# Kernel optimization log

Hardware: AMD Instinct MI355X
Metric: run time of the kernel (lower is better)

Reference implementation:

```python
import jax, jax.numpy as jnp
import numpy as np

B = 2          # graphs (images)
GRID = 13      # patches per spatial dim -> N = 169 patches per image
N = GRID * GRID
NN = B * N     # total nodes
C = 256        # hidden_dim / out_channels per head
H = 4          # attention heads
L = 3          # GAT layers
LRELU_SLOPE = 0.2
LN_EPS = 1e-5


def _dense_edges():
    # fully-connected directed graph (i != j) per image, as in create_graph
    idx = np.arange(N)
    src, dst = np.meshgrid(idx, idx, indexing='ij')
    mask = src != dst
    src, dst = src[mask], dst[mask]              # [N*(N-1)]
    offs = (np.arange(B) * N)[:, None]
    e_src = (src[None, :] + offs).reshape(-1)
    e_dst = (dst[None, :] + offs).reshape(-1)
    return e_src.astype(np.int32), e_dst.astype(np.int32)


def setup_inputs() -> dict:
    key = jax.random.key(0)
    ks = jax.random.split(key, 8)
    s = 0.05
    e_src, e_dst = _dense_edges()
    return {
        'x':   jax.random.normal(ks[0], (NN, C), jnp.float32),
        'Wl':  jax.random.normal(ks[1], (L, C, H * C), jnp.float32) * s,
        'bl':  jnp.zeros((L, H * C), jnp.float32),
        'Wr':  jax.random.normal(ks[2], (L, C, H * C), jnp.float32) * s,
        'br':  jnp.zeros((L, H * C), jnp.float32),
        'att': jax.random.normal(ks[3], (L, H, C), jnp.float32) * s,
        'bias': jnp.zeros((L, C), jnp.float32),
        'ln_g': jnp.ones((L, C), jnp.float32),
        'ln_b': jnp.zeros((L, C), jnp.float32),
        'W1':  jax.random.normal(ks[4], (L, C, 2 * C), jnp.float32) * s,
        'b1':  jnp.zeros((L, 2 * C), jnp.float32),
        'W2':  jax.random.normal(ks[5], (L, 2 * C, C), jnp.float32) * s,
        'b2':  jnp.zeros((L, C), jnp.float32),
        'edge_src': jnp.asarray(e_src),
        'edge_dst': jnp.asarray(e_dst),
        'batch_ids': jnp.repeat(jnp.arange(B, dtype=jnp.int32), N),
    }


def _gatv2(x, Wl, bl, Wr, br, att, bias, src, dst, n_nodes):
    # PyG GATv2Conv, concat=False (mean over heads)
    xl = (x @ Wl + bl).reshape(n_nodes, H, C)   # source transform
    xr = (x @ Wr + br).reshape(n_nodes, H, C)   # target transform
    e = jax.nn.leaky_relu(xl[src] + xr[dst], LRELU_SLOPE)     # [E,H,C]
    logits = jnp.einsum('ehc,hc->eh', e, att)                 # [E,H]
    m = jax.ops.segment_max(logits, dst, num_segments=n_nodes)
    a = jnp.exp(logits - m[dst])
    z = jax.ops.segment_sum(a, dst, num_segments=n_nodes)
    alpha = a / (z[dst] + 1e-16)                              # softmax per target
    msg = alpha[:, :, None] * xl[src]                         # [E,H,C]
    agg = jax.ops.segment_sum(msg, dst, num_segments=n_nodes) # [N,H,C]
    return agg.mean(axis=1) + bias


def _layernorm(x, g, b):
    mu = x.mean(-1, keepdims=True)
    var = jnp.mean((x - mu) ** 2, -1, keepdims=True)
    return (x - mu) * jax.lax.rsqrt(var + LN_EPS) * g + b


def reference(x, Wl, bl, Wr, br, att, bias, ln_g, ln_b, W1, b1, W2, b2,
              edge_src, edge_dst, batch_ids):
    n_nodes = x.shape[0]
    for l in range(L):
        residual = x
        h = _gatv2(x, Wl[l], bl[l], Wr[l], br[l], att[l], bias[l],
                   edge_src, edge_dst, n_nodes)
        h = _layernorm(h, ln_g[l], ln_b[l])
        mlp = jnp.maximum(h @ W1[l] + b1[l], 0.0) @ W2[l] + b2[l]
        x = residual + mlp
    # global mean pool per graph
    sums = jax.ops.segment_sum(x, batch_ids, num_segments=B)
    cnts = jax.ops.segment_sum(jnp.ones((n_nodes, 1), x.dtype), batch_ids,
                               num_segments=B)
    return sums / cnts
```

## Files before the change

kernel.cpp:

```cpp
#include <hip/hip_runtime.h>
#include <hip/hip_bf16.h>

typedef __hip_bfloat16 bf16;
typedef __attribute__((ext_vector_type(8))) short short8v;
typedef __attribute__((ext_vector_type(4))) float float4v;

#define NNODES 169
#define NNTOT  338
#define CH     256
#define NH     4
#define NL     3
#define SPAD   176
#define LN_EPS 1e-5f

__device__ __forceinline__ float b2f(bf16 v) { return __bfloat162float(v); }
__device__ __forceinline__ float lrelu(float v) { return fmaxf(v, 0.2f * v); }
__device__ __forceinline__ float ldm(const void* p, size_t i, int isbf) {
    return isbf ? b2f(((const bf16*)p)[i]) : ((const float*)p)[i];
}
__device__ __forceinline__ short f2bf(float f) {
    union { float f; unsigned u; } x; x.f = f;
    return (short)((x.u + 0x7FFFu + ((x.u >> 16) & 1u)) >> 16);
}
__device__ __forceinline__ int sniff_bf(const void* lng) {
    return ((((const unsigned*)lng)[0] & 0xFFFFu) == 0x3F80u) ? 1 : 0;
}

__global__ __launch_bounds__(256) void k_wt(
    const void* __restrict__ Wl, const void* __restrict__ Wr,
    const void* __restrict__ W1, const void* __restrict__ W2,
    short* __restrict__ wlT, short* __restrict__ wrT,
    short* __restrict__ w1T, short* __restrict__ w2T,
    const void* __restrict__ lng)
{
    __shared__ float s_t[32][33];
    const int isbf = sniff_bf(lng);
    const int z = blockIdx.z, mat = z & 3, l = z >> 2;
    const void* src; short* dst; int K, N;
    if      (mat == 0) { src = Wl; dst = wlT; K = CH;     N = NH * CH; }
    else if (mat == 1) { src = Wr; dst = wrT; K = CH;     N = NH * CH; }
    else if (mat == 2) { src = W1; dst = w1T; K = CH;     N = 2 * CH;  }
    else               { src = W2; dst = w2T; K = 2 * CH; N = CH;      }
    const int tiles = (K >> 5) * (N >> 5);
    if ((int)blockIdx.x >= tiles) return;
    const int tn = blockIdx.x % (N >> 5), tk = blockIdx.x / (N >> 5);
    const int k0 = tk * 32, n0 = tn * 32;
    const size_t lKN = (size_t)l * K * N;
    const int tx = threadIdx.x & 31, ty = threadIdx.x >> 5;

    for (int r = ty; r < 32; r += 8)
        s_t[r][tx] = ldm(src, lKN + (size_t)(k0 + r) * N + n0 + tx, isbf);
    __syncthreads();
    for (int r = ty; r < 32; r += 8)
        dst[lKN + (size_t)(n0 + r) * K + k0 + tx] = f2bf(s_t[tx][r]);
}

template<int ACT, int RES, int XLT>
__device__ __forceinline__ void mfma_gemm(
    const void* __restrict__ Av, int a_bf,
    const short* __restrict__ WT,
    const void* __restrict__ bv_, size_t oB, int isbf,
    const void* __restrict__ x_res, int r_bf,
    float* __restrict__ out, float* __restrict__ xlT,
    int M, int K, int N, int row0, int col0)
{
    __shared__ short sA[64 * 40];
    __shared__ short sBT[64 * 40];
    const int tid = threadIdx.x, lane = tid & 63, w = tid >> 6;
    const int arow = tid >> 2, akoff = (tid & 3) * 8;
    const int m = lane & 15, kb = (lane >> 4) * 8;
    const int w16 = w * 16;

    float4v acc[4];
    #pragma unroll
    for (int t = 0; t < 4; t++) acc[t] = (float4v){0.f, 0.f, 0.f, 0.f};

    for (int k0 = 0; k0 < K; k0 += 32) {
        short av8[8];
        const int gr = row0 + arow;
        if (gr < M) {
            const size_t ai = (size_t)gr * K + k0 + akoff;
            if (a_bf) {
                *(int4*)av8 = *(const int4*)((const bf16*)Av + ai);
            } else {
                const float4 f0 = *(const float4*)((const float*)Av + ai);
                const float4 f1 = *(const float4*)((const float*)Av + ai + 4);
                av8[0] = f2bf(f0.x); av8[1] = f2bf(f0.y);
                av8[2] = f2bf(f0.z); av8[3] = f2bf(f0.w);
                av8[4] = f2bf(f1.x); av8[5] = f2bf(f1.y);
                av8[6] = f2bf(f1.z); av8[7] = f2bf(f1.w);
            }
        } else {
            #pragma unroll
            for (int j = 0; j < 8; j++) av8[j] = 0;
        }
        short bv8[8];
        *(int4*)bv8 = *(const int4*)(WT + (size_t)(col0 + arow) * K + k0 + akoff);
        __syncthreads();
        *(short8v*)&sA[arow * 40 + akoff]  = *(short8v*)av8;
        *(short8v*)&sBT[arow * 40 + akoff] = *(short8v*)bv8;
        __syncthreads();
        const short8v af = *(const short8v*)&sA[(w16 + m) * 40 + kb];
        #pragma unroll
        for (int t = 0; t < 4; t++) {
            const short8v bf = *(const short8v*)&sBT[(t * 16 + m) * 40 + kb];
            acc[t] = __builtin_amdgcn_mfma_f32_16x16x32_bf16(af, bf, acc[t], 0, 0, 0);
        }
    }

    const int rq = (lane >> 4) * 4;
    #pragma unroll
    for (int t = 0; t < 4; t++) {
        const int col = col0 + t * 16 + m;
        const float bias_v = ldm(bv_, oB + col, isbf);
        #pragma unroll
        for (int r = 0; r < 4; r++) {
            const int gr = row0 + w16 + rq + r;
            if (gr >= M) continue;
            float v = acc[t][r] + bias_v;
            if (ACT) v = fmaxf(v, 0.f);
            if (RES) v += ldm(x_res, (size_t)gr * N + col, r_bf);
            out[(size_t)gr * N + col] = v;
            if (XLT) {
                const int hh = col >> 8, cc = col & 255;
                const int gg = (gr >= NNODES) ? 1 : 0;
                const int ss = gr - gg * NNODES;
                xlT[((size_t)(gg * NH + hh) * CH + cc) * SPAD + ss] = v;
            }
        }
    }
}

__global__ __launch_bounds__(256) void k_gemm_lr(
    const void* __restrict__ Av, int israw,
    const short* __restrict__ wlT, const short* __restrict__ wrT, size_t oWT,
    const void* __restrict__ bl, const void* __restrict__ br, size_t oB,
    float* __restrict__ xl, float* __restrict__ xr, float* __restrict__ xlT,
    const void* __restrict__ lng)
{
    const int isbf = sniff_bf(lng);
    const int a_bf = israw ? isbf : 0;
    const int row0 = blockIdx.x * 64, col0 = blockIdx.y * 64;
    if (blockIdx.z == 0)
        mfma_gemm<0,0,1>(Av, a_bf, wlT + oWT, bl, oB, isbf, nullptr, 0,
                         xl, xlT, NNTOT, CH, NH * CH, row0, col0);
    else
        mfma_gemm<0,0,0>(Av, a_bf, wrT + oWT, br, oB, isbf, nullptr, 0,
                         xr, nullptr, NNTOT, CH, NH * CH, row0, col0);
}

__global__ __launch_bounds__(256) void k_mlp1(
    const float* __restrict__ A, const short* __restrict__ w1T, size_t oWT,
    const void* __restrict__ b, size_t oB,
    float* __restrict__ out, const void* __restrict__ lng)
{
    const int isbf = sniff_bf(lng);
    mfma_gemm<1,0,0>(A, 0, w1T + oWT, b, oB, isbf, nullptr, 0,
                     out, nullptr, NNTOT, CH, 2 * CH, blockIdx.x * 64, blockIdx.y * 64);
}

__global__ __launch_bounds__(256) void k_mlp2(
    const float* __restrict__ A, const short* __restrict__ w2T, size_t oWT,
    const void* __restrict__ b, size_t oB,
    const void* __restrict__ x_res, int israw,
    float* __restrict__ out, const void* __restrict__ lng)
{
    const int isbf = sniff_bf(lng);
    const int r_bf = israw ? isbf : 0;
    mfma_gemm<0,1,0>(A, 0, w2T + oWT, b, oB, isbf, x_res, r_bf,
                     out, nullptr, NNTOT, 2 * CH, CH, blockIdx.x * 64, blockIdx.y * 64);
}

__global__ __launch_bounds__(256) void k_logits_sm(
    const float* __restrict__ xlT, const float* __restrict__ xr,
    const void* __restrict__ att, size_t oA,
    float* __restrict__ alphaR, const void* __restrict__ lng)
{
    __shared__ float s_att[CH];
    __shared__ float s_xr[4 * CH];
    __shared__ float s_tile[32 * SPAD];
    __shared__ float s_log[4 * SPAD];
    const int isbf = sniff_bf(lng);
    const int g = blockIdx.z, h = blockIdx.y, d0 = blockIdx.x * 4;
    const int tid = threadIdx.x, lane = tid & 63, wv = tid >> 6;

    s_att[tid] = ldm(att, oA + h * CH + tid, isbf);
    #pragma unroll
    for (int i = 0; i < 4; i++) {
        const int d = d0 + i;
        s_xr[i * CH + tid] = (d < NNODES)
            ? xr[(size_t)(g * NNODES + d) * (NH * CH) + h * CH + tid] : 0.f;
    }

    float l0 = 0.f, l1 = 0.f, l2 = 0.f, l3 = 0.f;
    const int s = tid;
    const float4* src = (const float4*)(xlT + ((size_t)(g * NH + h) * CH) * SPAD);
    for (int ch = 0; ch < 8; ch++) {
        __syncthreads();
        for (int i = tid; i < 32 * SPAD / 4; i += 256)
            ((float4*)s_tile)[i] = src[ch * (32 * SPAD / 4) + i];
        __syncthreads();
        if (s < NNODES) {
            const int cb = ch * 32;
            #pragma unroll
            for (int c = 0; c < 32; c++) {
                const float v = s_tile[c * SPAD + s];
                const float a = s_att[cb + c];
                l0 += a * lrelu(v + s_xr[cb + c]);
                l1 += a * lrelu(v + s_xr[CH + cb + c]);
                l2 += a * lrelu(v + s_xr[2 * CH + cb + c]);
                l3 += a * lrelu(v + s_xr[3 * CH + cb + c]);
            }
        }
    }
    if (s < NNODES) {
        s_log[s] = l0; s_log[SPAD + s] = l1;
        s_log[2 * SPAD + s] = l2; s_log[3 * SPAD + s] = l3;
    }
    __syncthreads();

    {
        const int d = d0 + wv;
        const float* row = s_log + wv * SPAD;
        const int s0 = lane, s1 = lane + 64, s2 = lane + 128;
        const float v0 = (s0 < NNODES && s0 != d) ? row[s0] : -1e30f;
        const float v1 = (s1 < NNODES && s1 != d) ? row[s1] : -1e30f;
        const float v2 = (s2 < NNODES && s2 != d) ? row[s2] : -1e30f;
        float mx = fmaxf(v0, fmaxf(v1, v2));
        mx = fmaxf(mx, __shfl_xor(mx, 32)); mx = fmaxf(mx, __shfl_xor(mx, 16));
        mx = fmaxf(mx, __shfl_xor(mx, 8));  mx = fmaxf(mx, __shfl_xor(mx, 4));
        mx = fmaxf(mx, __shfl_xor(mx, 2));  mx = fmaxf(mx, __shfl_xor(mx, 1));
        const float e0 = expf(v0 - mx), e1 = expf(v1 - mx), e2 = expf(v2 - mx);
        float z = e0 + e1 + e2;
        z += __shfl_xor(z, 32); z += __shfl_xor(z, 16); z += __shfl_xor(z, 8);
        z += __shfl_xor(z, 4);  z += __shfl_xor(z, 2);  z += __shfl_xor(z, 1);
        const float sc = 0.25f / (z + 1e-16f);
        if (d < NNODES) {
            float* arow = alphaR + ((size_t)(g * NH + h) * NNODES + d) * SPAD;
            if (s0 < NNODES) arow[s0] = e0 * sc;
            if (s1 < NNODES) arow[s1] = e1 * sc;
            if (s2 < NNODES) arow[s2] = e2 * sc;
        }
    }
}

__global__ __launch_bounds__(256) void k_agg(
    const float* __restrict__ alphaR, const float* __restrict__ xl,
    float* __restrict__ part)
{
    __shared__ float s_a[32 * 33];
    __shared__ float s_x[32 * 64];
    const int gh = blockIdx.z, g = gh >> 2, h = gh & 3;
    const int d0 = blockIdx.x * 32, c0 = blockIdx.y * 64;
    const int tid = threadIdx.x;
    const int dr = (tid >> 4) * 2, cq = (tid & 15) * 4;
    const int sr = tid >> 3, sc4 = (tid & 7) * 4;
    const int xc8 = (tid & 7) * 8;

    float acc[2][4] = {{0.f,0.f,0.f,0.f},{0.f,0.f,0.f,0.f}};

    for (int s0 = 0; s0 < NNODES; s0 += 32) {
        __syncthreads();
        {
            const int d = d0 + sr;
            const float* ap = alphaR + ((size_t)gh * NNODES + d) * SPAD + s0 + sc4;
            const int ok = (d < NNODES);
            s_a[sr * 33 + sc4 + 0] = (ok && s0 + sc4 + 0 < NNODES) ? ap[0] : 0.f;
            s_a[sr * 33 + sc4 + 1] = (ok && s0 + sc4 + 1 < NNODES) ? ap[1] : 0.f;
            s_a[sr * 33 + sc4 + 2] = (ok && s0 + sc4 + 2 < NNODES) ? ap[2] : 0.f;
            s_a[sr * 33 + sc4 + 3] = (ok && s0 + sc4 + 3 < NNODES) ? ap[3] : 0.f;
        }
        {
            const int sg = s0 + sr;
            if (sg < NNODES) {
                const float* xp = xl + (size_t)(g * NNODES + sg) * (NH * CH) + h * CH + c0 + xc8;
                *(float4*)&s_x[sr * 64 + xc8]     = *(const float4*)(xp);
                *(float4*)&s_x[sr * 64 + xc8 + 4] = *(const float4*)(xp + 4);
            } else {
                #pragma unroll
                for (int j = 0; j < 8; j++) s_x[sr * 64 + xc8 + j] = 0.f;
            }
        }
        __syncthreads();
        #pragma unroll
        for (int k = 0; k < 32; k++) {
            const float a0 = s_a[(dr + 0) * 33 + k];
            const float a1 = s_a[(dr + 1) * 33 + k];
            const float4 xv = *(const float4*)&s_x[k * 64 + cq];
            acc[0][0] += a0 * xv.x; acc[0][1] += a0 * xv.y;
            acc[0][2] += a0 * xv.z; acc[0][3] += a0 * xv.w;
            acc[1][0] += a1 * xv.x; acc[1][1] += a1 * xv.y;
            acc[1][2] += a1 * xv.z; acc[1][3] += a1 * xv.w;
        }
    }
    #pragma unroll
    for (int i = 0; i < 2; i++) {
        const int d = d0 + dr + i;
        if (d >= NNODES) continue;
        float4 v;
        v.x = acc[i][0]; v.y = acc[i][1]; v.z = acc[i][2]; v.w = acc[i][3];
        *(float4*)(part + ((size_t)h * NNTOT + g * NNODES + d) * CH + c0 + cq) = v;
    }
}

__global__ __launch_bounds__(256) void k_ln(
    const float* __restrict__ part,
    const void* __restrict__ bias, size_t oB,
    const void* __restrict__ ln_g, size_t oG,
    const void* __restrict__ ln_b, size_t oBt,
    float* __restrict__ h_out, const void* __restrict__ lng)
{
    __shared__ float s_red[8];
    const int isbf = sniff_bf(lng);
    const int node = blockIdx.x, c = threadIdx.x;
    const int lane = c & 63, wv = c >> 6;

    float vch = part[((size_t)0 * NNTOT + node) * CH + c]
              + part[((size_t)1 * NNTOT + node) * CH + c]
              + part[((size_t)2 * NNTOT + node) * CH + c]
              + part[((size_t)3 * NNTOT + node) * CH + c]
              + ldm(bias, oB + c, isbf);

    float s1 = vch, s2 = vch * vch;
    s1 += __shfl_xor(s1, 32); s2 += __shfl_xor(s2, 32);
    s1 += __shfl_xor(s1, 16); s2 += __shfl_xor(s2, 16);
    s1 += __shfl_xor(s1, 8);  s2 += __shfl_xor(s2, 8);
    s1 += __shfl_xor(s1, 4);  s2 += __shfl_xor(s2, 4);
    s1 += __shfl_xor(s1, 2);  s2 += __shfl_xor(s2, 2);
    s1 += __shfl_xor(s1, 1);  s2 += __shfl_xor(s2, 1);
    if (lane == 0) { s_red[wv] = s1; s_red[4 + wv] = s2; }
    __syncthreads();
    const float S1 = s_red[0] + s_red[1] + s_red[2] + s_red[3];
    const float S2 = s_red[4] + s_red[5] + s_red[6] + s_red[7];
    const float mu  = S1 * (1.f / CH);
    const float var = S2 * (1.f / CH) - mu * mu;
    const float o = (vch - mu) * rsqrtf(var + LN_EPS) * ldm(ln_g, oG + c, isbf)
                  + ldm(ln_b, oBt + c, isbf);
    h_out[(size_t)node * CH + c] = o;
}

__global__ __launch_bounds__(256) void k_pool(const float* __restrict__ x,
                                              void* __restrict__ out,
                                              const void* __restrict__ lng) {
    const int isbf = sniff_bf(lng);
    const int g = blockIdx.x, c = threadIdx.x;
    float s = 0.f;
    const float* p = x + (size_t)g * NNODES * CH + c;
    for (int n = 0; n < NNODES; n++) s += p[(size_t)n * CH];
    const float v = s * (1.f / NNODES);
    if (isbf) ((bf16*)out)[g * CH + c] = __float2bfloat16(v);
    else      ((float*)out)[g * CH + c] = v;
}

extern "C" void kernel_launch(void* const* d_in, const int* in_sizes, int n_in,
                              void* d_out, int out_size, void* d_ws, size_t ws_size,
                              hipStream_t stream)
{
    const void* x_in = d_in[0];
    const void* Wl   = d_in[1];
    const void* bl   = d_in[2];
    const void* Wr   = d_in[3];
    const void* br   = d_in[4];
    const void* att  = d_in[5];
    const void* bias = d_in[6];
    const void* lng  = d_in[7];
    const void* lnb  = d_in[8];
    const void* W1   = d_in[9];
    const void* b1   = d_in[10];
    const void* W2   = d_in[11];
    const void* b2   = d_in[12];

    float* ws     = (float*)d_ws;
    float* xl     = ws;
    float* xr     = xl + (size_t)NNTOT * NH * CH;
    float* xlT    = xr + (size_t)NNTOT * NH * CH;
    float* alphaR = xlT + (size_t)2 * NH * CH * SPAD;
    float* part   = alphaR + (size_t)2 * NH * NNODES * SPAD;
    float* h_ln   = part + (size_t)NH * NNTOT * CH;
    float* m1     = h_ln + (size_t)NNTOT * CH;
    float* xa     = m1 + (size_t)NNTOT * 2 * CH;
    float* xb     = xa + (size_t)NNTOT * CH;
    short* wlT    = (short*)(xb + (size_t)NNTOT * CH);
    short* wrT    = wlT + (size_t)NL * CH * NH * CH;
    short* w1T    = wrT + (size_t)NL * CH * NH * CH;
    short* w2T    = w1T + (size_t)NL * CH * 2 * CH;

    const size_t sB  = NH * CH;
    const size_t sA  = NH * CH;
    const size_t sC  = CH;
    const size_t sB1 = 2 * CH;
    const size_t sWT  = (size_t)CH * NH * CH;
    const size_t sW1T = (size_t)CH * 2 * CH;
    const size_t sW2T = (size_t)2 * CH * CH;

    k_wt<<<dim3(256, 1, 12), 256, 0, stream>>>(
        Wl, Wr, W1, W2, wlT, wrT, w1T, w2T, lng);

    const void* x_l[3] = { x_in, xa, xb };
    float*      x_o[3] = { xa, xb, xa };

    for (int l = 0; l < NL; l++) {
        const int israw = (l == 0);
        k_gemm_lr<<<dim3(6, 16, 2), 256, 0, stream>>>(
            x_l[l], israw, wlT, wrT, (size_t)l * sWT,
            bl, br, (size_t)l * sB, xl, xr, xlT, lng);
        k_logits_sm<<<dim3(43, NH, 2), 256, 0, stream>>>(
            xlT, xr, att, (size_t)l * sA, alphaR, lng);
        k_agg<<<dim3(6, 4, 8), 256, 0, stream>>>(alphaR, xl, part);
        k_ln<<<dim3(NNTOT), 256, 0, stream>>>(
            part, bias, (size_t)l * sC, lng, (size_t)l * sC, lnb, (size_t)l * sC,
            h_ln, lng);
        k_mlp1<<<dim3(6, 8), 256, 0, stream>>>(
            h_ln, w1T, (size_t)l * sW1T, b1, (size_t)l * sB1, m1, lng);
        k_mlp2<<<dim3(6, 4), 256, 0, stream>>>(
            m1, w2T, (size_t)l * sW2T, b2, (size_t)l * sC,
            x_l[l], israw, x_o[l], lng);
    }

    k_pool<<<dim3(2), 256, 0, stream>>>(xa, d_out, lng);
}
```

Baseline: 345.7 us.

## Fuse aggregation with layernorm, stage full-K GEMM tiles, widen logits chunks

```diff
diff --git a/kernel.cpp b/kernel.cpp
--- a/kernel.cpp
+++ b/kernel.cpp
@@ -55,56 +55,70 @@
         dst[lKN + (size_t)(n0 + r) * K + k0 + tx] = f2bf(s_t[tx][r]);
 }
 
-template<int ACT, int RES, int XLT>
+template<int KK, int ACT, int RES, int XLT>
 __device__ __forceinline__ void mfma_gemm(
+    short* __restrict__ sA, short* __restrict__ sBT,
     const void* __restrict__ Av, int a_bf,
     const short* __restrict__ WT,
     const void* __restrict__ bv_, size_t oB, int isbf,
     const void* __restrict__ x_res, int r_bf,
     float* __restrict__ out, float* __restrict__ xlT,
-    int M, int K, int N, int row0, int col0)
-{
-    __shared__ short sA[64 * 40];
-    __shared__ short sBT[64 * 40];
+    int M, int N, int row0, int col0)
+{
+    const int STR = KK + 8;
     const int tid = threadIdx.x, lane = tid & 63, w = tid >> 6;
-    const int arow = tid >> 2, akoff = (tid & 3) * 8;
+    const int r = tid >> 2, q = tid & 3;
+    const int kseg = KK / 4, kb0 = q * kseg;
     const int m = lane & 15, kb = (lane >> 4) * 8;
     const int w16 = w * 16;
+
+    {
+        const int gr = row0 + r;
+        const int ok = (gr < M);
+        if (a_bf) {
+            const bf16* ap = (const bf16*)Av + (size_t)gr * KK + kb0;
+            #pragma unroll
+            for (int j = 0; j < kseg; j += 8) {
+                int4 v = ok ? *(const int4*)(ap + j) : make_int4(0, 0, 0, 0);
+                *(int4*)&sA[r * STR + kb0 + j] = v;
+            }
+        } else {
+            const float* ap = (const float*)Av + (size_t)gr * KK + kb0;
+            #pragma unroll
+            for (int j = 0; j < kseg; j += 8) {
+                short v8[8];
+                if (ok) {
+                    const float4 f0 = *(const float4*)(ap + j);
+                    const float4 f1 = *(const float4*)(ap + j + 4);
+                    v8[0] = f2bf(f0.x); v8[1] = f2bf(f0.y);
+                    v8[2] = f2bf(f0.z); v8[3] = f2bf(f0.w);
+                    v8[4] = f2bf(f1.x); v8[5] = f2bf(f1.y);
+                    v8[6] = f2bf(f1.z); v8[7] = f2bf(f1.w);
+                } else {
+                    #pragma unroll
+                    for (int u = 0; u < 8; u++) v8[u] = 0;
+                }
+                *(int4*)&sA[r * STR + kb0 + j] = *(int4*)v8;
+            }
+        }
+        const short* bp = WT + (size_t)(col0 + r) * KK + kb0;
+        #pragma unroll
+        for (int j = 0; j < kseg; j += 8)
+            *(int4*)&sBT[r * STR + kb0 + j] = *(const int4*)(bp + j);
+    }
+    __syncthreads();
 
     float4v acc[4];
     #pragma unroll
     for (int t = 0; t < 4; t++) acc[t] = (float4v){0.f, 0.f, 0.f, 0.f};
 
-    for (int k0 = 0; k0 < K; k0 += 32) {
-        short av8[8];
-        const int gr = row0 + arow;
-        if (gr < M) {
-            const size_t ai = (size_t)gr * K + k0 + akoff;
-            if (a_bf) {
-                *(int4*)av8 = *(const int4*)((const bf16*)Av + ai);
-            } else {
-                const float4 f0 = *(const float4*)((const float*)Av + ai);
-                const float4 f1 = *(const float4*)((const float*)Av + ai + 4);
-                av8[0] = f2bf(f0.x); av8[1] = f2bf(f0.y);
-                av8[2] = f2bf(f0.z); av8[3] = f2bf(f0.w);
-                av8[4] = f2bf(f1.x); av8[5] = f2bf(f1.y);
-                av8[6] = f2bf(f1.z); av8[7] = f2bf(f1.w);
-            }
-        } else {
-            #pragma unroll
-            for (int j = 0; j < 8; j++) av8[j] = 0;
-        }
-        short bv8[8];
-        *(int4*)bv8 = *(const int4*)(WT + (size_t)(col0 + arow) * K + k0 + akoff);
-        __syncthreads();
-        *(short8v*)&sA[arow * 40 + akoff]  = *(short8v*)av8;
-        *(short8v*)&sBT[arow * 40 + akoff] = *(short8v*)bv8;
-        __syncthreads();
-        const short8v af = *(const short8v*)&sA[(w16 + m) * 40 + kb];
+    #pragma unroll
+    for (int kc = 0; kc < KK / 32; kc++) {
+        const short8v af = *(const short8v*)&sA[(w16 + m) * STR + kc * 32 + kb];
         #pragma unroll
         for (int t = 0; t < 4; t++) {
-            const short8v bf = *(const short8v*)&sBT[(t * 16 + m) * 40 + kb];
-            acc[t] = __builtin_amdgcn_mfma_f32_16x16x32_bf16(af, bf, acc[t], 0, 0, 0);
+            const short8v bfv = *(const short8v*)&sBT[(t * 16 + m) * STR + kc * 32 + kb];
+            acc[t] = __builtin_amdgcn_mfma_f32_16x16x32_bf16(af, bfv, acc[t], 0, 0, 0);
         }
     }
 
@@ -114,10 +128,10 @@
         const int col = col0 + t * 16 + m;
         const float bias_v = ldm(bv_, oB + col, isbf);
         #pragma unroll
-        for (int r = 0; r < 4; r++) {
-            const int gr = row0 + w16 + rq + r;
+        for (int rr = 0; rr < 4; rr++) {
+            const int gr = row0 + w16 + rq + rr;
             if (gr >= M) continue;
-            float v = acc[t][r] + bias_v;
+            float v = acc[t][rr] + bias_v;
             if (ACT) v = fmaxf(v, 0.f);
             if (RES) v += ldm(x_res, (size_t)gr * N + col, r_bf);
             out[(size_t)gr * N + col] = v;
@@ -138,15 +152,17 @@
     float* __restrict__ xl, float* __restrict__ xr, float* __restrict__ xlT,
     const void* __restrict__ lng)
 {
+    __shared__ short sA[64 * 264];
+    __shared__ short sBT[64 * 264];
     const int isbf = sniff_bf(lng);
     const int a_bf = israw ? isbf : 0;
     const int row0 = blockIdx.x * 64, col0 = blockIdx.y * 64;
     if (blockIdx.z == 0)
-        mfma_gemm<0,0,1>(Av, a_bf, wlT + oWT, bl, oB, isbf, nullptr, 0,
-                         xl, xlT, NNTOT, CH, NH * CH, row0, col0);
+        mfma_gemm<256,0,0,1>(sA, sBT, Av, a_bf, wlT + oWT, bl, oB, isbf,
+                             nullptr, 0, xl, xlT, NNTOT, NH * CH, row0, col0);
     else
-        mfma_gemm<0,0,0>(Av, a_bf, wrT + oWT, br, oB, isbf, nullptr, 0,
-                         xr, nullptr, NNTOT, CH, NH * CH, row0, col0);
+        mfma_gemm<256,0,0,0>(sA, sBT, Av, a_bf, wrT + oWT, br, oB, isbf,
+                             nullptr, 0, xr, nullptr, NNTOT, NH * CH, row0, col0);
 }
 
 __global__ __launch_bounds__(256) void k_mlp1(
@@ -154,9 +170,11 @@
     const void* __restrict__ b, size_t oB,
     float* __restrict__ out, const void* __restrict__ lng)
 {
-    const int isbf = sniff_bf(lng);
-    mfma_gemm<1,0,0>(A, 0, w1T + oWT, b, oB, isbf, nullptr, 0,
-                     out, nullptr, NNTOT, CH, 2 * CH, blockIdx.x * 64, blockIdx.y * 64);
+    __shared__ short sA[64 * 264];
+    __shared__ short sBT[64 * 264];
+    const int isbf = sniff_bf(lng);
+    mfma_gemm<256,1,0,0>(sA, sBT, A, 0, w1T + oWT, b, oB, isbf, nullptr, 0,
+                         out, nullptr, NNTOT, 2 * CH, blockIdx.x * 64, blockIdx.y * 64);
 }
 
 __global__ __launch_bounds__(256) void k_mlp2(
@@ -165,10 +183,12 @@
     const void* __restrict__ x_res, int israw,
     float* __restrict__ out, const void* __restrict__ lng)
 {
+    __shared__ short sA[64 * 520];
+    __shared__ short sBT[64 * 520];
     const int isbf = sniff_bf(lng);
     const int r_bf = israw ? isbf : 0;
-    mfma_gemm<0,1,0>(A, 0, w2T + oWT, b, oB, isbf, x_res, r_bf,
-                     out, nullptr, NNTOT, 2 * CH, CH, blockIdx.x * 64, blockIdx.y * 64);
+    mfma_gemm<512,0,1,0>(sA, sBT, A, 0, w2T + oWT, b, oB, isbf, x_res, r_bf,
+                         out, nullptr, NNTOT, CH, blockIdx.x * 64, blockIdx.y * 64);
 }
 
 __global__ __launch_bounds__(256) void k_logits_sm(
@@ -178,7 +198,7 @@
 {
     __shared__ float s_att[CH];
     __shared__ float s_xr[4 * CH];
-    __shared__ float s_tile[32 * SPAD];
+    __shared__ float s_tile[64 * SPAD];
     __shared__ float s_log[4 * SPAD];
     const int isbf = sniff_bf(lng);
     const int g = blockIdx.z, h = blockIdx.y, d0 = blockIdx.x * 4;
@@ -195,15 +215,15 @@
     float l0 = 0.f, l1 = 0.f, l2 = 0.f, l3 = 0.f;
     const int s = tid;
     const float4* src = (const float4*)(xlT + ((size_t)(g * NH + h) * CH) * SPAD);
-    for (int ch = 0; ch < 8; ch++) {
+    for (int ch = 0; ch < 4; ch++) {
         __syncthreads();
-        for (int i = tid; i < 32 * SPAD / 4; i += 256)
-            ((float4*)s_tile)[i] = src[ch * (32 * SPAD / 4) + i];
+        for (int i = tid; i < 64 * SPAD / 4; i += 256)
+            ((float4*)s_tile)[i] = src[ch * (64 * SPAD / 4) + i];
         __syncthreads();
         if (s < NNODES) {
-            const int cb = ch * 32;
-            #pragma unroll
-            for (int c = 0; c < 32; c++) {
+            const int cb = ch * 64;
+            #pragma unroll 8
+            for (int c = 0; c < 64; c++) {
                 const float v = s_tile[c * SPAD + s];
                 const float a = s_att[cb + c];
                 l0 += a * lrelu(v + s_xr[cb + c]);
@@ -244,99 +264,89 @@
     }
 }
 
-__global__ __launch_bounds__(256) void k_agg(
+__global__ __launch_bounds__(256) void k_aggln(
     const float* __restrict__ alphaR, const float* __restrict__ xl,
-    float* __restrict__ part)
-{
-    __shared__ float s_a[32 * 33];
-    __shared__ float s_x[32 * 64];
-    const int gh = blockIdx.z, g = gh >> 2, h = gh & 3;
-    const int d0 = blockIdx.x * 32, c0 = blockIdx.y * 64;
-    const int tid = threadIdx.x;
-    const int dr = (tid >> 4) * 2, cq = (tid & 15) * 4;
-    const int sr = tid >> 3, sc4 = (tid & 7) * 4;
-    const int xc8 = (tid & 7) * 8;
-
-    float acc[2][4] = {{0.f,0.f,0.f,0.f},{0.f,0.f,0.f,0.f}};
-
-    for (int s0 = 0; s0 < NNODES; s0 += 32) {
-        __syncthreads();
-        {
-            const int d = d0 + sr;
-            const float* ap = alphaR + ((size_t)gh * NNODES + d) * SPAD + s0 + sc4;
-            const int ok = (d < NNODES);
-            s_a[sr * 33 + sc4 + 0] = (ok && s0 + sc4 + 0 < NNODES) ? ap[0] : 0.f;
-            s_a[sr * 33 + sc4 + 1] = (ok && s0 + sc4 + 1 < NNODES) ? ap[1] : 0.f;
-            s_a[sr * 33 + sc4 + 2] = (ok && s0 + sc4 + 2 < NNODES) ? ap[2] : 0.f;
-            s_a[sr * 33 + sc4 + 3] = (ok && s0 + sc4 + 3 < NNODES) ? ap[3] : 0.f;
-        }
-        {
-            const int sg = s0 + sr;
-            if (sg < NNODES) {
-                const float* xp = xl + (size_t)(g * NNODES + sg) * (NH * CH) + h * CH + c0 + xc8;
-                *(float4*)&s_x[sr * 64 + xc8]     = *(const float4*)(xp);
-                *(float4*)&s_x[sr * 64 + xc8 + 4] = *(const float4*)(xp + 4);
-            } else {
-                #pragma unroll
-                for (int j = 0; j < 8; j++) s_x[sr * 64 + xc8 + j] = 0.f;
-            }
-        }
-        __syncthreads();
-        #pragma unroll
-        for (int k = 0; k < 32; k++) {
-            const float a0 = s_a[(dr + 0) * 33 + k];
-            const float a1 = s_a[(dr + 1) * 33 + k];
-            const float4 xv = *(const float4*)&s_x[k * 64 + cq];
-            acc[0][0] += a0 * xv.x; acc[0][1] += a0 * xv.y;
-            acc[0][2] += a0 * xv.z; acc[0][3] += a0 * xv.w;
-            acc[1][0] += a1 * xv.x; acc[1][1] += a1 * xv.y;
-            acc[1][2] += a1 * xv.z; acc[1][3] += a1 * xv.w;
-        }
-    }
-    #pragma unroll
-    for (int i = 0; i < 2; i++) {
-        const int d = d0 + dr + i;
-        if (d >= NNODES) continue;
-        float4 v;
-        v.x = acc[i][0]; v.y = acc[i][1]; v.z = acc[i][2]; v.w = acc[i][3];
-        *(float4*)(part + ((size_t)h * NNTOT + g * NNODES + d) * CH + c0 + cq) = v;
-    }
-}
-
-__global__ __launch_bounds__(256) void k_ln(
-    const float* __restrict__ part,
     const void* __restrict__ bias, size_t oB,
     const void* __restrict__ ln_g, size_t oG,
     const void* __restrict__ ln_b, size_t oBt,
     float* __restrict__ h_out, const void* __restrict__ lng)
 {
-    __shared__ float s_red[8];
-    const int isbf = sniff_bf(lng);
-    const int node = blockIdx.x, c = threadIdx.x;
-    const int lane = c & 63, wv = c >> 6;
-
-    float vch = part[((size_t)0 * NNTOT + node) * CH + c]
-              + part[((size_t)1 * NNTOT + node) * CH + c]
-              + part[((size_t)2 * NNTOT + node) * CH + c]
-              + part[((size_t)3 * NNTOT + node) * CH + c]
-              + ldm(bias, oB + c, isbf);
-
-    float s1 = vch, s2 = vch * vch;
-    s1 += __shfl_xor(s1, 32); s2 += __shfl_xor(s2, 32);
-    s1 += __shfl_xor(s1, 16); s2 += __shfl_xor(s2, 16);
-    s1 += __shfl_xor(s1, 8);  s2 += __shfl_xor(s2, 8);
-    s1 += __shfl_xor(s1, 4);  s2 += __shfl_xor(s2, 4);
-    s1 += __shfl_xor(s1, 2);  s2 += __shfl_xor(s2, 2);
-    s1 += __shfl_xor(s1, 1);  s2 += __shfl_xor(s2, 1);
-    if (lane == 0) { s_red[wv] = s1; s_red[4 + wv] = s2; }
+    __shared__ float s_alpha[16 * SPAD];
+    __shared__ float s_buf[16 * 1024];
+    const int isbf = sniff_bf(lng);
+    const int g = blockIdx.y, d0 = blockIdx.x * 4;
+    const int tid = threadIdx.x, lane = tid & 63, h = tid >> 6;
+    const int c4 = lane * 4;
+
+    for (int idx = tid; idx < 16 * SPAD; idx += 256) {
+        const int row = idx / SPAD, s = idx - row * SPAD;
+        const int hh = row >> 2, di = row & 3, d = d0 + di;
+        s_alpha[idx] = (d < NNODES && s < NNODES)
+            ? alphaR[((size_t)(g * NH + hh) * NNODES + d) * SPAD + s] : 0.f;
+    }
+
+    float4 A0 = {0,0,0,0}, A1 = {0,0,0,0}, A2 = {0,0,0,0}, A3 = {0,0,0,0};
+    for (int s0 = 0; s0 < NNODES; s0 += 16) {
+        __syncthreads();
+        for (int i = tid; i < 16 * 256; i += 256) {
+            const int si = i >> 8, cc = (i & 255) * 4;
+            const int s = s0 + si;
+            *(float4*)&s_buf[si * 1024 + cc] = (s < NNODES)
+                ? *(const float4*)(xl + (size_t)(g * NNODES + s) * 1024 + cc)
+                : make_float4(0.f, 0.f, 0.f, 0.f);
+        }
+        __syncthreads();
+        const int smax = min(16, NNODES - s0);
+        for (int si = 0; si < smax; si++) {
+            const float4 xv = *(const float4*)&s_buf[si * 1024 + h * 256 + c4];
+            const float a0 = s_alpha[(h * 4 + 0) * SPAD + s0 + si];
+            const float a1 = s_alpha[(h * 4 + 1) * SPAD + s0 + si];
+            const float a2 = s_alpha[(h * 4 + 2) * SPAD + s0 + si];
+            const float a3 = s_alpha[(h * 4 + 3) * SPAD + s0 + si];
+            A0.x += a0 * xv.x; A0.y += a0 * xv.y; A0.z += a0 * xv.z; A0.w += a0 * xv.w;
+            A1.x += a1 * xv.x; A1.y += a1 * xv.y; A1.z += a1 * xv.z; A1.w += a1 * xv.w;
+            A2.x += a2 * xv.x; A2.y += a2 * xv.y; A2.z += a2 * xv.z; A2.w += a2 * xv.w;
+            A3.x += a3 * xv.x; A3.y += a3 * xv.y; A3.z += a3 * xv.z; A3.w += a3 * xv.w;
+        }
+    }
     __syncthreads();
-    const float S1 = s_red[0] + s_red[1] + s_red[2] + s_red[3];
-    const float S2 = s_red[4] + s_red[5] + s_red[6] + s_red[7];
-    const float mu  = S1 * (1.f / CH);
-    const float var = S2 * (1.f / CH) - mu * mu;
-    const float o = (vch - mu) * rsqrtf(var + LN_EPS) * ldm(ln_g, oG + c, isbf)
-                  + ldm(ln_b, oBt + c, isbf);
-    h_out[(size_t)node * CH + c] = o;
+    *(float4*)&s_buf[(h * 4 + 0) * 256 + c4] = A0;
+    *(float4*)&s_buf[(h * 4 + 1) * 256 + c4] = A1;
+    *(float4*)&s_buf[(h * 4 + 2) * 256 + c4] = A2;
+    *(float4*)&s_buf[(h * 4 + 3) * 256 + c4] = A3;
+    __syncthreads();
+
+    {
+        const int d = d0 + h;
+        if (d < NNODES) {
+            float vch[4];
+            float s1 = 0.f, s2 = 0.f;
+            #pragma unroll
+            for (int j = 0; j < 4; j++) {
+                const float v = s_buf[(0 * 4 + h) * 256 + c4 + j]
+                              + s_buf[(1 * 4 + h) * 256 + c4 + j]
+                              + s_buf[(2 * 4 + h) * 256 + c4 + j]
+                              + s_buf[(3 * 4 + h) * 256 + c4 + j]
+                              + ldm(bias, oB + c4 + j, isbf);
+                vch[j] = v; s1 += v; s2 += v * v;
+            }
+            s1 += __shfl_xor(s1, 32); s2 += __shfl_xor(s2, 32);
+            s1 += __shfl_xor(s1, 16); s2 += __shfl_xor(s2, 16);
+            s1 += __shfl_xor(s1, 8);  s2 += __shfl_xor(s2, 8);
+            s1 += __shfl_xor(s1, 4);  s2 += __shfl_xor(s2, 4);
+            s1 += __shfl_xor(s1, 2);  s2 += __shfl_xor(s2, 2);
+            s1 += __shfl_xor(s1, 1);  s2 += __shfl_xor(s2, 1);
+            const float mu  = s1 * (1.f / CH);
+            const float var = s2 * (1.f / CH) - mu * mu;
+            const float rs  = rsqrtf(var + LN_EPS);
+            float4 o;
+            o.x = (vch[0] - mu) * rs * ldm(ln_g, oG + c4 + 0, isbf) + ldm(ln_b, oBt + c4 + 0, isbf);
+            o.y = (vch[1] - mu) * rs * ldm(ln_g, oG + c4 + 1, isbf) + ldm(ln_b, oBt + c4 + 1, isbf);
+            o.z = (vch[2] - mu) * rs * ldm(ln_g, oG + c4 + 2, isbf) + ldm(ln_b, oBt + c4 + 2, isbf);
+            o.w = (vch[3] - mu) * rs * ldm(ln_g, oG + c4 + 3, isbf) + ldm(ln_b, oBt + c4 + 3, isbf);
+            *(float4*)(h_out + (size_t)(g * NNODES + d) * CH + c4) = o;
+        }
+    }
 }
 
 __global__ __launch_bounds__(256) void k_pool(const float* __restrict__ x,
@@ -346,6 +356,7 @@
     const int g = blockIdx.x, c = threadIdx.x;
     float s = 0.f;
     const float* p = x + (size_t)g * NNODES * CH + c;
+    #pragma unroll 8
     for (int n = 0; n < NNODES; n++) s += p[(size_t)n * CH];
     const float v = s * (1.f / NNODES);
     if (isbf) ((bf16*)out)[g * CH + c] = __float2bfloat16(v);
@@ -375,8 +386,7 @@
     float* xr     = xl + (size_t)NNTOT * NH * CH;
     float* xlT    = xr + (size_t)NNTOT * NH * CH;
     float* alphaR = xlT + (size_t)2 * NH * CH * SPAD;
-    float* part   = alphaR + (size_t)2 * NH * NNODES * SPAD;
-    float* h_ln   = part + (size_t)NH * NNTOT * CH;
+    float* h_ln   = alphaR + (size_t)2 * NH * NNODES * SPAD;
     float* m1     = h_ln + (size_t)NNTOT * CH;
     float* xa     = m1 + (size_t)NNTOT * 2 * CH;
     float* xb     = xa + (size_t)NNTOT * CH;
@@ -406,10 +416,9 @@
             bl, br, (size_t)l * sB, xl, xr, xlT, lng);
         k_logits_sm<<<dim3(43, NH, 2), 256, 0, stream>>>(
             xlT, xr, att, (size_t)l * sA, alphaR, lng);
-        k_agg<<<dim3(6, 4, 8), 256, 0, stream>>>(alphaR, xl, part);
-        k_ln<<<dim3(NNTOT), 256, 0, stream>>>(
-            part, bias, (size_t)l * sC, lng, (size_t)l * sC, lnb, (size_t)l * sC,
-            h_ln, lng);
+        k_aggln<<<dim3(43, 2), 256, 0, stream>>>(
+            alphaR, xl, bias, (size_t)l * sC, lng, (size_t)l * sC,
+            lnb, (size_t)l * sC, h_ln, lng);
         k_mlp1<<<dim3(6, 8), 256, 0, stream>>>(
             h_ln, w1T, (size_t)l * sW1T, b1, (size_t)l * sB1, m1, lng);
         k_mlp2<<<dim3(6, 4), 256, 0, stream>>>(
```

Measured after the change: 525.9 us. 52.1% more time.
